# Performance work log

Hardware: AMD Instinct MI355X
Metric: run time of the kernel (lower is better)

The kernel has to match this reference:

```python
import jax, jax.numpy as jnp
import numpy as np

EPS = 1e-6
NUM_HEADS = 16


def _layernorm(x, g, b):
    m = jnp.mean(x, axis=-1, keepdims=True)
    v = jnp.mean(jnp.square(x - m), axis=-1, keepdims=True)
    return (x - m) * jax.lax.rsqrt(v + EPS) * g + b


def setup_inputs() -> dict:
    key = jax.random.key(0)
    ks = jax.random.split(key, 16)
    B, Lq, Lkv, D = 2, 2048, 4096, 2048
    Hd = D // NUM_HEADS
    s = 0.02
    return {
        "hidden_states": jax.random.normal(ks[0], (B, Lq, D), jnp.float32),
        "cross_attention_states": jax.random.normal(ks[1], (B, Lkv, D), jnp.float32),
        "q_w": jax.random.normal(ks[2], (D, D), jnp.float32) * s,
        "q_b": jnp.zeros((D,), jnp.float32),
        "k_w": jax.random.normal(ks[3], (D, D), jnp.float32) * s,
        "k_b": jnp.zeros((D,), jnp.float32),
        "v_w": jax.random.normal(ks[4], (D, D), jnp.float32) * s,
        "v_b": jnp.zeros((D,), jnp.float32),
        "o_w": jax.random.normal(ks[5], (D, D), jnp.float32) * s,
        "o_b": jnp.zeros((D,), jnp.float32),
        "qn_g": jnp.ones((Hd,), jnp.float32),
        "qn_b": jnp.zeros((Hd,), jnp.float32),
        "kn_g": jnp.ones((Hd,), jnp.float32),
        "kn_b": jnp.zeros((Hd,), jnp.float32),
    }


def reference(hidden_states, cross_attention_states,
              q_w, q_b, k_w, k_b, v_w, v_b, o_w, o_b,
              qn_g, qn_b, kn_g, kn_b):
    B, Lq, D = hidden_states.shape
    H = NUM_HEADS
    Hd = D // H
    scale = Hd ** -0.5

    # torch Linear: y = x @ W^T + b
    q = hidden_states @ q_w.T + q_b                        # [B,Lq,D]
    k = cross_attention_states @ k_w.T + k_b               # [B,Lkv,D]
    v = cross_attention_states @ v_w.T + v_b               # [B,Lkv,D]

    q = q.reshape(B, Lq, H, Hd).transpose(0, 2, 1, 3)      # [B,H,Lq,Hd]
    k = k.reshape(B, -1, H, Hd).transpose(0, 2, 1, 3)      # [B,H,Lkv,Hd]
    v = v.reshape(B, -1, H, Hd).transpose(0, 2, 1, 3)      # [B,H,Lkv,Hd]

    # per-head QK LayerNorm before scores
    q = _layernorm(q, qn_g, qn_b)
    k = _layernorm(k, kn_g, kn_b)

    attn_weights = jnp.einsum('bhqd,bhkd->bhqk', q, k) * scale
    attn_weights = jax.nn.softmax(attn_weights.astype(jnp.float32), axis=-1).astype(q.dtype)
    # dropout p=0.0 (inference) -> identity

    attn_output = jnp.einsum('bhqk,bhkd->bhqd', attn_weights, v)
    attn_output = attn_output.transpose(0, 2, 1, 3).reshape(B, Lq, D)
    attn_output = attn_output @ o_w.T + o_b
    return attn_output, attn_weights
```

## Files before the change

### kernel.cpp

```cpp
#include <hip/hip_runtime.h>
#include <cstdint>
#include <cstddef>

using u16 = unsigned short;
using f32x4 = __attribute__((ext_vector_type(4))) float;
using bf8   = __attribute__((ext_vector_type(8))) short;

#define DEVFN __device__ __forceinline__

constexpr int BB  = 2;
constexpr int LQ  = 2048;
constexpr int LKV = 4096;
constexpr int DD  = 2048;
constexpr int NH  = 16;
constexpr int HDm = 128;
constexpr float ATTN_SCALE = 0.08838834764831845f;
constexpr float LN_EPS = 1e-6f;
constexpr float LOG2E  = 1.4426950408889634f;
constexpr float SHIFT2 = 17.312340490667562f;

DEVFN u16 f2bf(float f) {
  unsigned u = __builtin_bit_cast(unsigned, f);
  u += 0x7fffu + ((u >> 16) & 1u);
  return (u16)(u >> 16);
}
DEVFN float bf2f(u16 h) { return __builtin_bit_cast(float, (unsigned)h << 16); }
DEVFN f32x4 mfma16(bf8 a, bf8 b, f32x4 c) {
  return __builtin_amdgcn_mfma_f32_16x16x32_bf16(a, b, c, 0, 0, 0);
}
DEVFN void gl16(const void* g, void* l) {
  __builtin_amdgcn_global_load_lds(
      (const __attribute__((address_space(1))) void*)g,
      (__attribute__((address_space(3))) void*)l, 16, 0, 0);
}
DEVFN void barrier_hard() {
  __builtin_amdgcn_s_barrier();
  __builtin_amdgcn_sched_barrier(0);
}

__global__ __launch_bounds__(256) void k_cvt(const float4* __restrict__ in,
                                             ushort4* __restrict__ out, int n4) {
  int i = blockIdx.x * 256 + threadIdx.x;
  if (i >= n4) return;
  float4 v = in[i];
  ushort4 o;
  o.x = f2bf(v.x); o.y = f2bf(v.y); o.z = f2bf(v.z); o.w = f2bf(v.w);
  out[i] = o;
}

template <int MODE>
__global__ __launch_bounds__(256) void k_gemm_nt(const u16* __restrict__ X,
                                                 const u16* __restrict__ Wt,
                                                 const float* __restrict__ bias,
                                                 const float* __restrict__ lng,
                                                 const float* __restrict__ lnb,
                                                 void* __restrict__ Y,
                                                 int M, int N, int K) {
  __shared__ __align__(16) u16 As[128 * 64];
  __shared__ __align__(16) u16 Bs[128 * 64];
  __shared__ float Sm[2][128], Sq[2][128];
  const int tid = threadIdx.x;
  const int w = tid >> 6, l = tid & 63;
  const int m0 = blockIdx.x * 128, n0 = blockIdx.y * 128;
  const int wr = w >> 1, wc = w & 1;
  const int lr = l & 15, lk = (l >> 4) * 8;
  const int rsw = (l & 7) << 3;
  const int srow = l >> 3;
  const int scb = (l & 7) * 16;
  f32x4 acc[4][4] = {};

  for (int k0 = 0; k0 < K; k0 += 64) {
#pragma unroll
    for (int i = 0; i < 4; ++i) {
      int rbase = w * 32 + i * 8;
      int row = rbase + srow;
      int cb = scb ^ ((row & 7) << 4);
      gl16((const char*)&X[(size_t)(m0 + row) * K + k0] + cb, &As[rbase * 64]);
      gl16((const char*)&Wt[(size_t)(n0 + row) * K + k0] + cb, &Bs[rbase * 64]);
    }
    __syncthreads();
    bf8 af[4][2], bfr[4][2];
#pragma unroll
    for (int mi = 0; mi < 4; ++mi)
#pragma unroll
      for (int kk = 0; kk < 2; ++kk)
        af[mi][kk] = *(const bf8*)&As[(wr * 64 + mi * 16 + lr) * 64 + ((kk * 32 + lk) ^ rsw)];
#pragma unroll
    for (int ni = 0; ni < 4; ++ni)
#pragma unroll
      for (int kk = 0; kk < 2; ++kk)
        bfr[ni][kk] = *(const bf8*)&Bs[(wc * 64 + ni * 16 + lr) * 64 + ((kk * 32 + lk) ^ rsw)];
#pragma unroll
    for (int kk = 0; kk < 2; ++kk)
#pragma unroll
      for (int mi = 0; mi < 4; ++mi)
#pragma unroll
        for (int ni = 0; ni < 4; ++ni)
          acc[mi][ni] = mfma16(af[mi][kk], bfr[ni][kk], acc[mi][ni]);
    __syncthreads();
  }
  const int lrg = (l >> 4) * 4;

  float bv[4];
#pragma unroll
  for (int ni = 0; ni < 4; ++ni) bv[ni] = bias[n0 + wc * 64 + ni * 16 + lr];
#pragma unroll
  for (int mi = 0; mi < 4; ++mi)
#pragma unroll
    for (int ni = 0; ni < 4; ++ni)
#pragma unroll
      for (int r = 0; r < 4; ++r) acc[mi][ni][r] += bv[ni];

  if constexpr (MODE >= 2) {
#pragma unroll
    for (int mi = 0; mi < 4; ++mi) {
#pragma unroll
      for (int r = 0; r < 4; ++r) {
        float ps = 0.f, pq = 0.f;
#pragma unroll
        for (int ni = 0; ni < 4; ++ni) {
          float v = acc[mi][ni][r];
          ps += v; pq += v * v;
        }
#pragma unroll
        for (int m = 1; m < 16; m <<= 1) {
          ps += __shfl_xor(ps, m);
          pq += __shfl_xor(pq, m);
        }
        if (lr == 0) {
          int rl = wr * 64 + mi * 16 + lrg + r;
          Sm[wc][rl] = ps; Sq[wc][rl] = pq;
        }
      }
    }
    __syncthreads();
    float gv[4], bbv[4];
#pragma unroll
    for (int ni = 0; ni < 4; ++ni) {
      int c = wc * 64 + ni * 16 + lr;
      gv[ni] = lng[c]; bbv[ni] = lnb[c];
    }
#pragma unroll
    for (int mi = 0; mi < 4; ++mi)
#pragma unroll
      for (int r = 0; r < 4; ++r) {
        int rl = wr * 64 + mi * 16 + lrg + r;
        float mean = (Sm[0][rl] + Sm[1][rl]) * (1.f / 128.f);
        float var  = (Sq[0][rl] + Sq[1][rl]) * (1.f / 128.f) - mean * mean;
        float rs = rsqrtf(var + LN_EPS);
#pragma unroll
        for (int ni = 0; ni < 4; ++ni) {
          float o = (acc[mi][ni][r] - mean) * rs * gv[ni] + bbv[ni];
          if (MODE == 3) o *= ATTN_SCALE;
          acc[mi][ni][r] = o;
        }
      }
  }

#pragma unroll
  for (int ni = 0; ni < 4; ++ni) {
    int n = n0 + wc * 64 + ni * 16 + lr;
#pragma unroll
    for (int mi = 0; mi < 4; ++mi) {
      int mb = m0 + wr * 64 + mi * 16 + lrg;
#pragma unroll
      for (int r = 0; r < 4; ++r) {
        float v = acc[mi][ni][r];
        if constexpr (MODE == 1)
          __builtin_nontemporal_store(v, &((float*)Y)[(size_t)(mb + r) * N + n]);
        else
          ((u16*)Y)[(size_t)(mb + r) * N + n] = f2bf(v);
      }
    }
  }
}

__global__ __launch_bounds__(256) void k_vtrans(const u16* __restrict__ V,
                                                u16* __restrict__ Vt) {
  int bh = blockIdx.y;
  int b = bh >> 4, h = bh & 15;
  int kv0 = blockIdx.x * 64;
  __shared__ __align__(16) u16 t[64][136];
  int tid = threadIdx.x;
  int r = tid >> 4, c = (tid & 15) * 8;
#pragma unroll
  for (int i = 0; i < 4; ++i) {
    int row = i * 16 + r;
    *(int4*)&t[row][c] = *(const int4*)&V[((size_t)b * LKV + kv0 + row) * DD + h * HDm + c];
  }
  __syncthreads();
  int hd_ = tid >> 3, kvc = (tid & 7) * 8;
#pragma unroll
  for (int i = 0; i < 4; ++i) {
    int hd = i * 32 + hd_;
    u16 tmp[8] __attribute__((aligned(16)));
#pragma unroll
    for (int j = 0; j < 8; ++j) tmp[j] = t[kvc + j][hd];
    *(int4*)&Vt[((size_t)bh * HDm + hd) * LKV + kv0 + kvc] = *(const int4*)tmp;
  }
}

__global__ __launch_bounds__(512, 4) void k_attn(const u16* __restrict__ Qp,
                                                 const u16* __restrict__ Kp,
                                                 const u16* __restrict__ Vt,
                                                 float* __restrict__ Wout,
                                                 u16* __restrict__ AO) {
  const int g = blockIdx.x;
  const int work = (g & 7) * 64 + (g >> 3);
  const int bh = work >> 4;
  const int b = bh >> 4, h = bh & 15;
  const int q0 = (work & 15) * 128;
  const int tid = threadIdx.x, w = tid >> 6, l = tid & 63;
  const int lr = l & 15, lk = (l >> 4) * 8, lrg = (l >> 4) * 4;
  const int rsw = (l & 7) << 3;
  __shared__ __align__(16) u16 Ks[2][64 * 128];
  __shared__ __align__(16) u16 Vs[2][128 * 64];
  __shared__ __align__(16) u16 Ps[8][16 * 64];

  bf8 qf[4];
  {
    const u16* qb = &Qp[((size_t)b * LQ + q0 + w * 16 + lr) * DD + h * HDm];
#pragma unroll
    for (int kc = 0; kc < 4; ++kc) qf[kc] = *(const bf8*)(qb + kc * 32 + lk);
  }
  const u16* Kb = Kp + (size_t)b * LKV * DD + h * HDm;
  const u16* Vb = Vt + (size_t)bh * HDm * LKV;

  auto stageK = [&](int buf, int kv0) {
#pragma unroll
    for (int i = 0; i < 2; ++i) {
      int rbase = i * 32 + w * 4;
      int row = rbase + (l >> 4);
      int cb = ((l & 15) * 16) ^ ((row & 7) << 4);
      gl16((const char*)(Kb + (size_t)(kv0 + row) * DD) + cb, &Ks[buf][rbase * 128]);
    }
  };
  auto stageV = [&](int buf, int kv0) {
#pragma unroll
    for (int i = 0; i < 2; ++i) {
      int rbase = i * 64 + w * 8;
      int row = rbase + (l >> 3);
      int cb = ((l & 7) * 16) ^ ((row & 7) << 4);
      gl16((const char*)(Vb + (size_t)row * LKV + kv0) + cb, &Vs[buf][rbase * 64]);
    }
  };

  float lsum[4] = {0.f, 0.f, 0.f, 0.f};
  stageK(0, 0);
  asm volatile("s_waitcnt vmcnt(0)" ::: "memory");
  barrier_hard();
  for (int t = 0; t < 64; ++t) {
    const int cur = t & 1;
    if (t < 63) stageK(cur ^ 1, (t + 1) * 64);
    f32x4 s[4];
    __builtin_amdgcn_s_setprio(1);
#pragma unroll
    for (int ni = 0; ni < 4; ++ni) {
      s[ni] = f32x4{0.f, 0.f, 0.f, 0.f};
#pragma unroll
      for (int kc = 0; kc < 4; ++kc) {
        bf8 kf = *(const bf8*)&Ks[cur][(ni * 16 + lr) * 128 + ((kc * 32 + lk) ^ rsw)];
        s[ni] = mfma16(qf[kc], kf, s[ni]);
      }
    }
    __builtin_amdgcn_s_setprio(0);
#pragma unroll
    for (int ni = 0; ni < 4; ++ni)
#pragma unroll
      for (int r = 0; r < 4; ++r)
        lsum[r] += exp2f(fmaf(s[ni][r], LOG2E, -SHIFT2));
    asm volatile("s_waitcnt vmcnt(0)" ::: "memory");
    barrier_hard();
  }
  float inv[4];
#pragma unroll
  for (int r = 0; r < 4; ++r) {
    float v = lsum[r];
#pragma unroll
    for (int m = 1; m < 16; m <<= 1) v += __shfl_xor(v, m);
    inv[r] = 1.f / v;
  }

  f32x4 oacc[8] = {};
  stageK(0, 0); stageV(0, 0);
  asm volatile("s_waitcnt vmcnt(0)" ::: "memory");
  barrier_hard();
  float* wbase = Wout + ((size_t)bh * LQ + q0 + w * 16 + lrg) * LKV;
  for (int t = 0; t < 64; ++t) {
    const int cur = t & 1;
    const int kv0 = t * 64;
    if (t < 63) {
      stageK(cur ^ 1, kv0 + 64);
      stageV(cur ^ 1, kv0 + 64);
    }
    f32x4 s[4];
    __builtin_amdgcn_s_setprio(1);
#pragma unroll
    for (int ni = 0; ni < 4; ++ni) {
      s[ni] = f32x4{0.f, 0.f, 0.f, 0.f};
#pragma unroll
      for (int kc = 0; kc < 4; ++kc) {
        bf8 kf = *(const bf8*)&Ks[cur][(ni * 16 + lr) * 128 + ((kc * 32 + lk) ^ rsw)];
        s[ni] = mfma16(qf[kc], kf, s[ni]);
      }
    }
    __builtin_amdgcn_s_setprio(0);
#pragma unroll
    for (int ni = 0; ni < 4; ++ni) {
#pragma unroll
      for (int r = 0; r < 4; ++r) {
        float p = exp2f(fmaf(s[ni][r], LOG2E, -SHIFT2)) * inv[r];
        __builtin_nontemporal_store(p, &wbase[(size_t)r * LKV + kv0 + ni * 16 + lr]);
        int row = lrg + r;
        Ps[w][row * 64 + ((ni * 16 + lr) ^ ((row & 7) << 3))] = f2bf(p);
      }
    }
    asm volatile("s_waitcnt lgkmcnt(0)" ::: "memory");
    __builtin_amdgcn_sched_barrier(0);
    __builtin_amdgcn_s_setprio(1);
#pragma unroll
    for (int kk = 0; kk < 2; ++kk) {
      bf8 pf = *(const bf8*)&Ps[w][lr * 64 + ((kk * 32 + lk) ^ rsw)];
#pragma unroll
      for (int c = 0; c < 8; ++c) {
        bf8 vf = *(const bf8*)&Vs[cur][(c * 16 + lr) * 64 + ((kk * 32 + lk) ^ rsw)];
        oacc[c] = mfma16(pf, vf, oacc[c]);
      }
    }
    __builtin_amdgcn_s_setprio(0);
    asm volatile("s_waitcnt vmcnt(16)" ::: "memory");
    barrier_hard();
  }
#pragma unroll
  for (int c = 0; c < 8; ++c)
#pragma unroll
    for (int r = 0; r < 4; ++r)
      AO[((size_t)b * LQ + q0 + w * 16 + lrg + r) * DD + h * HDm + c * 16 + lr] =
          f2bf(oacc[c][r]);
}

extern "C" void kernel_launch(void* const* d_in, const int* in_sizes, int n_in,
                              void* d_out, int out_size, void* d_ws, size_t ws_size,
                              hipStream_t stream) {
  const float* hs   = (const float*)d_in[0];
  const float* cas  = (const float*)d_in[1];
  const float* q_w  = (const float*)d_in[2];
  const float* q_b  = (const float*)d_in[3];
  const float* k_w  = (const float*)d_in[4];
  const float* k_b  = (const float*)d_in[5];
  const float* v_w  = (const float*)d_in[6];
  const float* v_b  = (const float*)d_in[7];
  const float* o_w  = (const float*)d_in[8];
  const float* o_b  = (const float*)d_in[9];
  const float* qn_g = (const float*)d_in[10];
  const float* qn_b = (const float*)d_in[11];
  const float* kn_g = (const float*)d_in[12];
  const float* kn_b = (const float*)d_in[13];

  float* out_attn = (float*)d_out;
  float* out_w    = out_attn + (size_t)BB * LQ * DD;

  constexpr size_t SZ_Q  = (size_t)BB * LQ * DD * 2;
  constexpr size_t SZ_KV = (size_t)BB * LKV * DD * 2;
  constexpr size_t SZ_W  = (size_t)DD * DD * 2;
  char* p = (char*)d_ws;
  u16* hsb  = (u16*)p;              p += SZ_Q;
  u16* casb = (u16*)p;              p += SZ_KV;
  u16* qwb  = (u16*)p;              p += SZ_W;
  u16* kwb  = (u16*)p;              p += SZ_W;
  u16* vwb  = (u16*)p;              p += SZ_W;
  u16* owb  = (u16*)p;              p += SZ_W;
  u16* Qp   = (u16*)p;              p += SZ_Q;
  u16* Kp   = (u16*)p;              p += SZ_KV;
  u16* Vp   = (u16*)p;              p += SZ_KV;
  u16* Vtp  = (u16*)p;              p += SZ_KV;
  u16* AO   = (u16*)p;              p += SZ_Q;

  auto cvt = [&](const float* src, u16* dst, size_t n) {
    int n4 = (int)(n / 4);
    k_cvt<<<dim3((n4 + 255) / 256), dim3(256), 0, stream>>>(
        (const float4*)src, (ushort4*)dst, n4);
  };
  cvt(hs,  hsb,  (size_t)BB * LQ * DD);
  cvt(cas, casb, (size_t)BB * LKV * DD);
  cvt(q_w, qwb, (size_t)DD * DD);
  cvt(k_w, kwb, (size_t)DD * DD);
  cvt(v_w, vwb, (size_t)DD * DD);
  cvt(o_w, owb, (size_t)DD * DD);

  k_gemm_nt<3><<<dim3(BB * LQ / 128, DD / 128), dim3(256), 0, stream>>>(
      hsb, qwb, q_b, qn_g, qn_b, Qp, BB * LQ, DD, DD);
  k_gemm_nt<2><<<dim3(BB * LKV / 128, DD / 128), dim3(256), 0, stream>>>(
      casb, kwb, k_b, kn_g, kn_b, Kp, BB * LKV, DD, DD);
  k_gemm_nt<0><<<dim3(BB * LKV / 128, DD / 128), dim3(256), 0, stream>>>(
      casb, vwb, v_b, nullptr, nullptr, Vp, BB * LKV, DD, DD);

  k_vtrans<<<dim3(LKV / 64, BB * NH), dim3(256), 0, stream>>>(Vp, Vtp);

  k_attn<<<dim3(LQ / 128 * BB * NH), dim3(512), 0, stream>>>(Qp, Kp, Vtp, out_w, AO);

  k_gemm_nt<1><<<dim3(BB * LQ / 128, DD / 128), dim3(256), 0, stream>>>(
      AO, owb, o_b, nullptr, nullptr, out_attn, BB * LQ, DD, DD);
}
```

Measured before the change: 777.8 us.

## Fuse V transpose into V-projection GEMM and software-pipeline attention QK tiles

The V projection GEMM gets a new epilogue mode that transposes its tile through shared memory and writes V directly in the per-head transposed layout. This removes the separate transpose kernel and the intermediate V buffer round trip. The attention kernel now double-buffers score tiles, computing the QK product for the next tile while finishing exp/store/PV for the previous one. It also folds the softmax normalization into the exponent as a log offset, replacing a multiply by the reciprocal. Register pressure rises from holding two score tiles, and the GEMM epilogue adds a shared-memory pass.

```diff
diff --git a/kernel.cpp b/kernel.cpp
--- a/kernel.cpp
+++ b/kernel.cpp
@@ -56,9 +56,10 @@
                                                  const float* __restrict__ lnb,
                                                  void* __restrict__ Y,
                                                  int M, int N, int K) {
-  __shared__ __align__(16) u16 As[128 * 64];
-  __shared__ __align__(16) u16 Bs[128 * 64];
+  __shared__ __align__(16) u16 Sh[2][128 * 64];
   __shared__ float Sm[2][128], Sq[2][128];
+  u16* As = Sh[0];
+  u16* Bs = Sh[1];
   const int tid = threadIdx.x;
   const int w = tid >> 6, l = tid & 63;
   const int m0 = blockIdx.x * 128, n0 = blockIdx.y * 128;
@@ -111,7 +112,7 @@
 #pragma unroll
       for (int r = 0; r < 4; ++r) acc[mi][ni][r] += bv[ni];
 
-  if constexpr (MODE >= 2) {
+  if constexpr (MODE == 2 || MODE == 3) {
 #pragma unroll
     for (int mi = 0; mi < 4; ++mi) {
 #pragma unroll
@@ -157,6 +158,37 @@
       }
   }
 
+  if constexpr (MODE == 4) {
+    u16* T = &Sh[0][0];
+#pragma unroll
+    for (int mi = 0; mi < 4; ++mi)
+#pragma unroll
+      for (int ni = 0; ni < 4; ++ni)
+#pragma unroll
+        for (int r = 0; r < 4; ++r) {
+          int mrow = wr * 64 + mi * 16 + lrg + r;
+          int ncol = wc * 64 + ni * 16 + lr;
+          T[mrow * 128 + (ncol ^ ((mrow & 7) << 3))] = f2bf(acc[mi][ni][r]);
+        }
+    __syncthreads();
+    int hd = tid >> 1, half = tid & 1;
+    int bq = m0 >> 12;
+    int kvb = (m0 & (LKV - 1)) + half * 64;
+    int hh = n0 >> 7;
+    u16* vout = (u16*)Y + ((size_t)(bq * NH + hh) * HDm + hd) * LKV + kvb;
+#pragma unroll
+    for (int j8 = 0; j8 < 8; ++j8) {
+      u16 tmp[8] __attribute__((aligned(16)));
+#pragma unroll
+      for (int j = 0; j < 8; ++j) {
+        int kv = half * 64 + j8 * 8 + j;
+        tmp[j] = T[kv * 128 + (hd ^ ((kv & 7) << 3))];
+      }
+      *(int4*)&vout[j8 * 8] = *(const int4*)tmp;
+    }
+    return;
+  }
+
 #pragma unroll
   for (int ni = 0; ni < 4; ++ni) {
     int n = n0 + wc * 64 + ni * 16 + lr;
@@ -172,31 +204,6 @@
           ((u16*)Y)[(size_t)(mb + r) * N + n] = f2bf(v);
       }
     }
-  }
-}
-
-__global__ __launch_bounds__(256) void k_vtrans(const u16* __restrict__ V,
-                                                u16* __restrict__ Vt) {
-  int bh = blockIdx.y;
-  int b = bh >> 4, h = bh & 15;
-  int kv0 = blockIdx.x * 64;
-  __shared__ __align__(16) u16 t[64][136];
-  int tid = threadIdx.x;
-  int r = tid >> 4, c = (tid & 15) * 8;
-#pragma unroll
-  for (int i = 0; i < 4; ++i) {
-    int row = i * 16 + r;
-    *(int4*)&t[row][c] = *(const int4*)&V[((size_t)b * LKV + kv0 + row) * DD + h * HDm + c];
-  }
-  __syncthreads();
-  int hd_ = tid >> 3, kvc = (tid & 7) * 8;
-#pragma unroll
-  for (int i = 0; i < 4; ++i) {
-    int hd = i * 32 + hd_;
-    u16 tmp[8] __attribute__((aligned(16)));
-#pragma unroll
-    for (int j = 0; j < 8; ++j) tmp[j] = t[kvc + j][hd];
-    *(int4*)&Vt[((size_t)bh * HDm + hd) * LKV + kv0 + kvc] = *(const int4*)tmp;
   }
 }
 
@@ -244,72 +251,70 @@
       gl16((const char*)(Vb + (size_t)row * LKV + kv0) + cb, &Vs[buf][rbase * 64]);
     }
   };
+  auto qk_tile = [&](int t, f32x4 (&s)[4]) {
+    const u16* ks = Ks[t & 1];
+    __builtin_amdgcn_s_setprio(1);
+#pragma unroll
+    for (int ni = 0; ni < 4; ++ni) {
+      s[ni] = f32x4{0.f, 0.f, 0.f, 0.f};
+#pragma unroll
+      for (int kc = 0; kc < 4; ++kc) {
+        bf8 kf = *(const bf8*)&ks[(ni * 16 + lr) * 128 + ((kc * 32 + lk) ^ rsw)];
+        s[ni] = mfma16(qf[kc], kf, s[ni]);
+      }
+    }
+    __builtin_amdgcn_s_setprio(0);
+  };
 
   float lsum[4] = {0.f, 0.f, 0.f, 0.f};
+  auto sumexp = [&](const f32x4 (&s)[4]) {
+#pragma unroll
+    for (int ni = 0; ni < 4; ++ni)
+#pragma unroll
+      for (int r = 0; r < 4; ++r)
+        lsum[r] += exp2f(fmaf(s[ni][r], LOG2E, -SHIFT2));
+  };
+  f32x4 sA[4], sB[4];
   stageK(0, 0);
   asm volatile("s_waitcnt vmcnt(0)" ::: "memory");
   barrier_hard();
-  for (int t = 0; t < 64; ++t) {
-    const int cur = t & 1;
-    if (t < 63) stageK(cur ^ 1, (t + 1) * 64);
-    f32x4 s[4];
-    __builtin_amdgcn_s_setprio(1);
-#pragma unroll
-    for (int ni = 0; ni < 4; ++ni) {
-      s[ni] = f32x4{0.f, 0.f, 0.f, 0.f};
-#pragma unroll
-      for (int kc = 0; kc < 4; ++kc) {
-        bf8 kf = *(const bf8*)&Ks[cur][(ni * 16 + lr) * 128 + ((kc * 32 + lk) ^ rsw)];
-        s[ni] = mfma16(qf[kc], kf, s[ni]);
-      }
-    }
-    __builtin_amdgcn_s_setprio(0);
-#pragma unroll
-    for (int ni = 0; ni < 4; ++ni)
-#pragma unroll
-      for (int r = 0; r < 4; ++r)
-        lsum[r] += exp2f(fmaf(s[ni][r], LOG2E, -SHIFT2));
+  stageK(1, 64);
+  qk_tile(0, sA);
+  asm volatile("s_waitcnt vmcnt(0)" ::: "memory");
+  barrier_hard();
+  for (int t = 1; t < 64; t += 2) {
+    if (t < 63) stageK((t + 1) & 1, (t + 1) * 64);
+    qk_tile(t, sB);
+    sumexp(sA);
     asm volatile("s_waitcnt vmcnt(0)" ::: "memory");
     barrier_hard();
-  }
-  float inv[4];
+    if (t + 1 < 64) {
+      if (t + 1 < 63) stageK((t + 2) & 1, (t + 2) * 64);
+      qk_tile(t + 1, sA);
+      sumexp(sB);
+      asm volatile("s_waitcnt vmcnt(0)" ::: "memory");
+      barrier_hard();
+    }
+  }
+  sumexp(sB);
+  float cr[4];
 #pragma unroll
   for (int r = 0; r < 4; ++r) {
     float v = lsum[r];
 #pragma unroll
     for (int m = 1; m < 16; m <<= 1) v += __shfl_xor(v, m);
-    inv[r] = 1.f / v;
+    cr[r] = -(SHIFT2 + __log2f(v));
   }
 
   f32x4 oacc[8] = {};
-  stageK(0, 0); stageV(0, 0);
-  asm volatile("s_waitcnt vmcnt(0)" ::: "memory");
-  barrier_hard();
   float* wbase = Wout + ((size_t)bh * LQ + q0 + w * 16 + lrg) * LKV;
-  for (int t = 0; t < 64; ++t) {
-    const int cur = t & 1;
-    const int kv0 = t * 64;
-    if (t < 63) {
-      stageK(cur ^ 1, kv0 + 64);
-      stageV(cur ^ 1, kv0 + 64);
-    }
-    f32x4 s[4];
-    __builtin_amdgcn_s_setprio(1);
+  auto finish = [&](int tp, const f32x4 (&s)[4]) {
+    const int kv0 = tp * 64;
 #pragma unroll
     for (int ni = 0; ni < 4; ++ni) {
-      s[ni] = f32x4{0.f, 0.f, 0.f, 0.f};
-#pragma unroll
-      for (int kc = 0; kc < 4; ++kc) {
-        bf8 kf = *(const bf8*)&Ks[cur][(ni * 16 + lr) * 128 + ((kc * 32 + lk) ^ rsw)];
-        s[ni] = mfma16(qf[kc], kf, s[ni]);
-      }
-    }
-    __builtin_amdgcn_s_setprio(0);
-#pragma unroll
-    for (int ni = 0; ni < 4; ++ni) {
 #pragma unroll
       for (int r = 0; r < 4; ++r) {
-        float p = exp2f(fmaf(s[ni][r], LOG2E, -SHIFT2)) * inv[r];
+        float p = exp2f(fmaf(s[ni][r], LOG2E, cr[r]));
         __builtin_nontemporal_store(p, &wbase[(size_t)r * LKV + kv0 + ni * 16 + lr]);
         int row = lrg + r;
         Ps[w][row * 64 + ((ni * 16 + lr) ^ ((row & 7) << 3))] = f2bf(p);
@@ -323,14 +328,38 @@
       bf8 pf = *(const bf8*)&Ps[w][lr * 64 + ((kk * 32 + lk) ^ rsw)];
 #pragma unroll
       for (int c = 0; c < 8; ++c) {
-        bf8 vf = *(const bf8*)&Vs[cur][(c * 16 + lr) * 64 + ((kk * 32 + lk) ^ rsw)];
+        bf8 vf = *(const bf8*)&Vs[tp & 1][(c * 16 + lr) * 64 + ((kk * 32 + lk) ^ rsw)];
         oacc[c] = mfma16(pf, vf, oacc[c]);
       }
     }
     __builtin_amdgcn_s_setprio(0);
+  };
+
+  stageK(0, 0);
+  asm volatile("s_waitcnt vmcnt(0)" ::: "memory");
+  barrier_hard();
+  stageK(1, 64); stageV(0, 0);
+  qk_tile(0, sA);
+  asm volatile("s_waitcnt vmcnt(0)" ::: "memory");
+  barrier_hard();
+  for (int t = 1; t < 64; t += 2) {
+    if (t < 63) stageK((t + 1) & 1, (t + 1) * 64);
+    stageV(t & 1, t * 64);
+    qk_tile(t, sB);
+    finish(t - 1, sA);
     asm volatile("s_waitcnt vmcnt(16)" ::: "memory");
     barrier_hard();
-  }
+    if (t + 1 < 64) {
+      if (t + 1 < 63) stageK((t + 2) & 1, (t + 2) * 64);
+      stageV((t + 1) & 1, (t + 1) * 64);
+      qk_tile(t + 1, sA);
+      finish(t, sB);
+      asm volatile("s_waitcnt vmcnt(16)" ::: "memory");
+      barrier_hard();
+    }
+  }
+  finish(63, sB);
+
 #pragma unroll
   for (int c = 0; c < 8; ++c)
 #pragma unroll
@@ -372,7 +401,6 @@
   u16* owb  = (u16*)p;              p += SZ_W;
   u16* Qp   = (u16*)p;              p += SZ_Q;
   u16* Kp   = (u16*)p;              p += SZ_KV;
-  u16* Vp   = (u16*)p;              p += SZ_KV;
   u16* Vtp  = (u16*)p;              p += SZ_KV;
   u16* AO   = (u16*)p;              p += SZ_Q;
 
@@ -392,10 +420,8 @@
       hsb, qwb, q_b, qn_g, qn_b, Qp, BB * LQ, DD, DD);
   k_gemm_nt<2><<<dim3(BB * LKV / 128, DD / 128), dim3(256), 0, stream>>>(
       casb, kwb, k_b, kn_g, kn_b, Kp, BB * LKV, DD, DD);
-  k_gemm_nt<0><<<dim3(BB * LKV / 128, DD / 128), dim3(256), 0, stream>>>(
-      casb, vwb, v_b, nullptr, nullptr, Vp, BB * LKV, DD, DD);
-
-  k_vtrans<<<dim3(LKV / 64, BB * NH), dim3(256), 0, stream>>>(Vp, Vtp);
+  k_gemm_nt<4><<<dim3(BB * LKV / 128, DD / 128), dim3(256), 0, stream>>>(
+      casb, vwb, v_b, nullptr, nullptr, Vtp, BB * LKV, DD, DD);
 
   k_attn<<<dim3(LQ / 128 * BB * NH), dim3(512), 0, stream>>>(Qp, Kp, Vtp, out_w, AO);
 
```

New measurement: 790.0 us. Within noise of the previous version (+1.6%).
